# Performance work log

Hardware: AMD Instinct MI355X
Metric: run time of the kernel (lower is better)

The kernel has to match this reference:

```python
import jax, jax.numpy as jnp
import numpy as np

B, N, D = 1, 2048, 1024
L, H, DH = 4, 16, 64
INNER = H * DH            # 1024, == D
FF = int(D * 4.0)         # 4096 (GEGLU inner)
SCALE = DH ** -0.5
LN_EPS = 1e-5


def setup_inputs() -> dict:
    key = jax.random.key(0)
    ks = jax.random.split(key, 8)
    w = 0.02
    inp = {
        'x': jax.random.normal(ks[0], (B, N, D), jnp.float32),
        'mask': jnp.ones((B, N), dtype=bool),
        # stacked per-layer params (leading dim L)
        'Wqkv': jax.random.normal(ks[1], (L, D, 3 * INNER), jnp.float32) * w,
        'Wo': jax.random.normal(ks[2], (L, INNER, D), jnp.float32) * w,
        'bo': jnp.zeros((L, D), jnp.float32),
        'ln1_g': jnp.ones((L, D), jnp.float32),
        'ln1_b': jnp.zeros((L, D), jnp.float32),
        'ln2_g': jnp.ones((L, D), jnp.float32),
        'ln2_b': jnp.zeros((L, D), jnp.float32),
        'ls1': jnp.full((L, D), 0.1, jnp.float32),  # LayerScale init_eps=0.1 (depth<=18)
        'ls2': jnp.full((L, D), 0.1, jnp.float32),
        'W1': jax.random.normal(ks[3], (L, D, 2 * FF), jnp.float32) * w,
        'b1': jnp.zeros((L, 2 * FF), jnp.float32),
        'W2': jax.random.normal(ks[4], (L, FF, D), jnp.float32) * w,
        'b2': jnp.zeros((L, D), jnp.float32),
    }
    return inp


def _layernorm(x, g, b):
    mu = jnp.mean(x, axis=-1, keepdims=True)
    var = jnp.mean(jnp.square(x - mu), axis=-1, keepdims=True)
    return (x - mu) * jax.lax.rsqrt(var + LN_EPS) * g + b


def _forward(x, mask, Wqkv, Wo, bo, ln1_g, ln1_b, ln2_g, ln2_b, ls1, ls2, W1, b1, W2, b2):
    n = x.shape[1]
    causal = jnp.arange(n)[None, :] > jnp.arange(n)[:, None]  # True = masked
    valid = mask[:, None, None, :] & ~causal[None, None]       # (B,1,N,N) True = keep
    for l in range(L):
        # --- attention sublayer: x + LayerScale(PreNorm(Attn))(x) ---
        h = _layernorm(x, ln1_g[l], ln1_b[l])
        qkv = h @ Wqkv[l]                                      # (B,N,3*INNER)
        q, k, v = jnp.split(qkv, 3, axis=-1)
        q = q.reshape(B, n, H, DH).transpose(0, 2, 1, 3) * SCALE
        k = k.reshape(B, n, H, DH).transpose(0, 2, 1, 3)
        v = v.reshape(B, n, H, DH).transpose(0, 2, 1, 3)
        dots = jnp.einsum('bhid,bhjd->bhij', q, k)             # (B,H,N,N)
        neg = -jnp.finfo(dots.dtype).max
        dots = jnp.where(valid, dots, neg)
        attn = jax.nn.softmax(dots, axis=-1)                   # stable_softmax, temp=1
        o = jnp.einsum('bhij,bhjd->bhid', attn, v)
        o = o.transpose(0, 2, 1, 3).reshape(B, n, INNER)
        o = o @ Wo[l] + bo[l]
        x = x + o * ls1[l]
        # --- feedforward sublayer: x + LayerScale(PreNorm(GEGLU-FFN))(x) ---
        h = _layernorm(x, ln2_g[l], ln2_b[l])
        u = h @ W1[l] + b1[l]                                  # (B,N,2*FF)
        a, g = jnp.split(u, 2, axis=-1)
        f = (a * jax.nn.gelu(g, approximate=False)) @ W2[l] + b2[l]
        x = x + f * ls2[l]
    return x


def reference(x, mask, Wqkv, Wo, bo, ln1_g, ln1_b, ln2_g, ln2_b, ls1, ls2, W1, b1, W2, b2):
    return _forward(x, mask, Wqkv, Wo, bo, ln1_g, ln1_b, ln2_g, ln2_b, ls1, ls2, W1, b1, W2, b2)
```

## Files before the change

### kernel.cpp

```cpp
#include <hip/hip_runtime.h>
#include <hip/hip_bf16.h>
#include <math.h>

#define LN_EPS 1e-5f
#define ATT_SCALE 0.125f

typedef __bf16 bf16x8 __attribute__((ext_vector_type(8)));
typedef float f32x4 __attribute__((ext_vector_type(4)));

__device__ __forceinline__ unsigned short f2bf(float f){
  unsigned int u = __builtin_bit_cast(unsigned int, f);
  u += 0x7fffu + ((u >> 16) & 1u);
  return (unsigned short)(u >> 16);
}
__device__ __forceinline__ float bfbits2f(unsigned int lo16){
  return __builtin_bit_cast(float, lo16 << 16);
}

__global__ __launch_bounds__(256) void ln_kernel(
    const float* __restrict__ X, const float* __restrict__ g,
    const float* __restrict__ b, unsigned short* __restrict__ H)
{
  __shared__ float red[4];
  int row = blockIdx.x, t = threadIdx.x;
  const float4 xv = ((const float4*)(X + (size_t)row*1024))[t];
  float s = xv.x + xv.y + xv.z + xv.w;
  #pragma unroll
  for (int o=32;o;o>>=1) s += __shfl_down(s,o);
  if ((t&63)==0) red[t>>6] = s;
  __syncthreads();
  float mu = (red[0]+red[1]+red[2]+red[3]) * (1.f/1024.f);
  __syncthreads();
  float dx = xv.x-mu, dy = xv.y-mu, dz = xv.z-mu, dw = xv.w-mu;
  float s2 = dx*dx+dy*dy+dz*dz+dw*dw;
  #pragma unroll
  for (int o=32;o;o>>=1) s2 += __shfl_down(s2,o);
  if ((t&63)==0) red[t>>6] = s2;
  __syncthreads();
  float var = (red[0]+red[1]+red[2]+red[3]) * (1.f/1024.f);
  float rs = rsqrtf(var + LN_EPS);
  const float4 gv = ((const float4*)g)[t];
  const float4 bv = ((const float4*)b)[t];
  ushort4 o4;
  o4.x = f2bf(dx*rs*gv.x + bv.x);
  o4.y = f2bf(dy*rs*gv.y + bv.y);
  o4.z = f2bf(dz*rs*gv.z + bv.z);
  o4.w = f2bf(dw*rs*gv.w + bv.w);
  ((ushort4*)(H + (size_t)row*1024))[t] = o4;
}

template<int SK, int DO_LN>
__global__ __launch_bounds__(256) void redln_kernel(
    const float* __restrict__ P, float* __restrict__ X,
    const float* __restrict__ bias, const float* __restrict__ scale,
    const float* __restrict__ g, const float* __restrict__ b,
    unsigned short* __restrict__ H)
{
  __shared__ float red[4];
  int row = blockIdx.x, t = threadIdx.x;
  size_t off = (size_t)row*1024 + t*4;
  float4 xv = *(const float4*)(X + off);
  float4 pv = *(const float4*)(P + off);
  #pragma unroll
  for (int c=1;c<SK;c++){
    float4 q = *(const float4*)(P + (size_t)c*2048*1024 + off);
    pv.x+=q.x; pv.y+=q.y; pv.z+=q.z; pv.w+=q.w;
  }
  const float4 bv = ((const float4*)bias)[t];
  const float4 sv = ((const float4*)scale)[t];
  xv.x += (pv.x+bv.x)*sv.x;
  xv.y += (pv.y+bv.y)*sv.y;
  xv.z += (pv.z+bv.z)*sv.z;
  xv.w += (pv.w+bv.w)*sv.w;
  *(float4*)(X + off) = xv;
  if (DO_LN){
    float s = xv.x + xv.y + xv.z + xv.w;
    #pragma unroll
    for (int o=32;o;o>>=1) s += __shfl_down(s,o);
    if ((t&63)==0) red[t>>6] = s;
    __syncthreads();
    float mu = (red[0]+red[1]+red[2]+red[3]) * (1.f/1024.f);
    __syncthreads();
    float dx = xv.x-mu, dy = xv.y-mu, dz = xv.z-mu, dw = xv.w-mu;
    float s2 = dx*dx+dy*dy+dz*dz+dw*dw;
    #pragma unroll
    for (int o=32;o;o>>=1) s2 += __shfl_down(s2,o);
    if ((t&63)==0) red[t>>6] = s2;
    __syncthreads();
    float var = (red[0]+red[1]+red[2]+red[3]) * (1.f/1024.f);
    float rs = rsqrtf(var + LN_EPS);
    const float4 gv = ((const float4*)g)[t];
    const float4 lbv = ((const float4*)b)[t];
    ushort4 o4;
    o4.x = f2bf(dx*rs*gv.x + lbv.x);
    o4.y = f2bf(dy*rs*gv.y + lbv.y);
    o4.z = f2bf(dz*rs*gv.z + lbv.z);
    o4.w = f2bf(dw*rs*gv.w + lbv.w);
    ((ushort4*)(H + (size_t)row*1024))[t] = o4;
  }
}

__global__ __launch_bounds__(256) void trc_kernel(
    const float* __restrict__ W, unsigned short* __restrict__ WT, int K, int N)
{
  __shared__ float tile[64][65];
  int n0 = blockIdx.x*64, k0 = blockIdx.y*64;
  int t = threadIdx.x;
  int tx = t & 63, ty = t >> 6;
  #pragma unroll
  for (int p=0;p<16;p++){
    int r = ty*16+p;
    tile[r][tx] = W[(size_t)(k0+r)*N + n0 + tx];
  }
  __syncthreads();
  int kc = t & 31, tb = t >> 5;
  #pragma unroll
  for (int p=0;p<8;p++){
    int nr = tb + p*8;
    unsigned int lo = f2bf(tile[2*kc][nr]);
    unsigned int hi = f2bf(tile[2*kc+1][nr]);
    ((unsigned int*)(WT + (size_t)(n0+nr)*K + k0))[kc] = lo | (hi<<16);
  }
}

template<int MODE>
__global__ __launch_bounds__(256) void gemm_bt(
    const unsigned short* __restrict__ A, const unsigned short* __restrict__ BT,
    int M, int N, int K,
    float* __restrict__ Xres, unsigned short* __restrict__ Obf,
    const float* __restrict__ bias, const float* __restrict__ scale)
{
  __shared__ unsigned short Asm[128*64];
  __shared__ unsigned short Bsm[128*64];
  int t = threadIdx.x;
  int lane = t & 63;
  int w = t >> 6, wm = w >> 1, wn = w & 1;

  int nwg = gridDim.x * gridDim.y;
  int wg = blockIdx.y * gridDim.x + blockIdx.x;
  int cpx = nwg >> 3;
  int swz = (wg & 7) * cpx + (wg >> 3);
  int bn = swz % gridDim.x, bm = swz / gridDim.x;

  f32x4 acc[4][4] = {};
  int ktBeg = 0, ktEnd = K >> 6;
  if (MODE == 3){
    int per = (K >> 6) / gridDim.z;
    ktBeg = blockIdx.z * per;
    ktEnd = ktBeg + per;
  }

  for (int kt = ktBeg; kt < ktEnd; ++kt){
    #pragma unroll
    for (int c=0;c<4;c++){
      int li = c*256 + t;
      int row = li >> 3, sc = li & 7;
      int gc = sc ^ (row & 7);
      const unsigned short* sa = A  + (size_t)(bm*128 + row)*K + kt*64 + gc*8;
      const unsigned short* sb = BT + (size_t)(bn*128 + row)*K + kt*64 + gc*8;
      __builtin_amdgcn_global_load_lds(
        (const __attribute__((address_space(1))) unsigned int*)sa,
        (__attribute__((address_space(3))) unsigned int*)(Asm + (size_t)(c*256 + (t & ~63))*8),
        16, 0, 0);
      __builtin_amdgcn_global_load_lds(
        (const __attribute__((address_space(1))) unsigned int*)sb,
        (__attribute__((address_space(3))) unsigned int*)(Bsm + (size_t)(c*256 + (t & ~63))*8),
        16, 0, 0);
    }
    __syncthreads();
    #pragma unroll
    for (int kk=0;kk<2;kk++){
      bf16x8 aF[4], bF[4];
      #pragma unroll
      for (int m=0;m<4;m++){
        int row = wm*64 + m*16 + (lane&15);
        int ch = kk*4 + (lane>>4);
        aF[m] = *(const bf16x8*)&Asm[row*64 + (ch ^ (row&7))*8];
      }
      #pragma unroll
      for (int n=0;n<4;n++){
        int row = wn*64 + n*16 + (lane&15);
        int ch = kk*4 + (lane>>4);
        bF[n] = *(const bf16x8*)&Bsm[row*64 + (ch ^ (row&7))*8];
      }
      #pragma unroll
      for (int m=0;m<4;m++)
        #pragma unroll
        for (int n=0;n<4;n++)
          acc[m][n] = __builtin_amdgcn_mfma_f32_16x16x32_bf16(aF[m], bF[n], acc[m][n], 0,0,0);
    }
    __syncthreads();
  }

  int colg = lane & 15;
  #pragma unroll
  for (int m=0;m<4;m++){
    int gr0 = bm*128 + wm*64 + m*16 + (lane>>4)*4;
    #pragma unroll
    for (int n=0;n<4;n++){
      int gc = bn*128 + wn*64 + n*16 + colg;
      #pragma unroll
      for (int j=0;j<4;j++){
        int gr = gr0 + j;
        float v = acc[m][n][j];
        if (MODE==0){
          Obf[(size_t)gr*N + gc] = f2bf(v);
        } else if (MODE==1){
          Obf[(size_t)gr*N + gc] = f2bf(v + bias[gc]);
        } else if (MODE==2){
          size_t idx = (size_t)gr*N + gc;
          Xres[idx] = Xres[idx] + (v + bias[gc]) * scale[gc];
        } else {
          Xres[(size_t)blockIdx.z*((size_t)M*N) + (size_t)gr*N + gc] = v;
        }
      }
    }
  }
}

__global__ __launch_bounds__(256) void vtr_kernel(
    const unsigned short* __restrict__ qkv, unsigned short* __restrict__ VT)
{
  __shared__ unsigned int tile[64][33];
  int h = blockIdx.y;
  int n0 = blockIdx.x * 64;
  int t = threadIdx.x;
  #pragma unroll
  for (int p=0;p<8;p++){
    int idx = p*256 + t;
    int r = idx >> 5, c = idx & 31;
    tile[r][c] = *(const unsigned int*)(qkv + (size_t)(n0+r)*3072 + 2048 + h*64 + c*2);
  }
  __syncthreads();
  #pragma unroll
  for (int p=0;p<8;p++){
    int idx = p*256 + t;
    int d = idx >> 5, c = idx & 31;
    unsigned int a = tile[2*c][d>>1];
    unsigned int b = tile[2*c+1][d>>1];
    unsigned int lo = (d&1) ? (a>>16) : (a & 0xffffu);
    unsigned int hi = (d&1) ? (b>>16) : (b & 0xffffu);
    *(unsigned int*)(VT + (size_t)h*131072 + (size_t)d*2048 + n0 + c*2) = lo | (hi<<16);
  }
}

__global__ __launch_bounds__(256) void flash_attn(
    const unsigned short* __restrict__ qkv,
    const unsigned short* __restrict__ VT,
    unsigned short* __restrict__ O)
{
  __shared__ unsigned short Klds[64*64];
  __shared__ unsigned short Vlds[64*64];
  __shared__ unsigned short Plds[4][16*72];
  __shared__ float fbuf[4][16];
  __shared__ float lbuf[4][16];

  int t = threadIdx.x;
  int lane = t & 63;
  int w = t >> 6;
  int q15 = lane & 15, l16 = lane >> 4;

  int bid = blockIdx.x;
  int half = bid >> 8, idx = bid & 255;
  int h = (idx >> 5) + half*8;
  int qt = half ? (31 - (idx & 31)) : (idx & 31);
  int q0 = qt * 64;

  bf16x8 qF[2];
  int qrow = q0 + w*16 + q15;
  #pragma unroll
  for (int db=0; db<2; db++)
    qF[db] = *(const bf16x8*)(qkv + (size_t)qrow*3072 + h*64 + db*32 + l16*8);

  f32x4 o[4] = {};
  float m_run = -1e30f, l_run = 0.f;

  for (int kt = 0; kt <= qt; ++kt){
    int k0 = kt*64;
    #pragma unroll
    for (int c=0;c<2;c++){
      int li = c*256 + t;
      int row = li >> 3, sc = li & 7;
      int gc = sc ^ (row & 7);
      const unsigned short* sk = qkv + (size_t)(k0+row)*3072 + 1024 + h*64 + gc*8;
      const unsigned short* sv = VT + (size_t)h*131072 + (size_t)row*2048 + k0 + gc*8;
      __builtin_amdgcn_global_load_lds(
        (const __attribute__((address_space(1))) unsigned int*)sk,
        (__attribute__((address_space(3))) unsigned int*)(Klds + (c*256 + (t & ~63))*8),
        16, 0, 0);
      __builtin_amdgcn_global_load_lds(
        (const __attribute__((address_space(1))) unsigned int*)sv,
        (__attribute__((address_space(3))) unsigned int*)(Vlds + (c*256 + (t & ~63))*8),
        16, 0, 0);
    }
    __syncthreads();

    f32x4 s[4] = {};
    #pragma unroll
    for (int km=0;km<4;km++){
      #pragma unroll
      for (int db=0;db<2;db++){
        int row = km*16 + q15;
        int ch = db*4 + l16;
        bf16x8 kF = *(const bf16x8*)&Klds[row*64 + (ch ^ (row&7))*8];
        s[km] = __builtin_amdgcn_mfma_f32_16x16x32_bf16(kF, qF[db], s[km], 0,0,0);
      }
    }

    bool diag = (kt == qt);
    float pmax = -1e30f;
    #pragma unroll
    for (int km=0;km<4;km++){
      #pragma unroll
      for (int j=0;j<4;j++){
        float sv = s[km][j] * ATT_SCALE;
        if (diag){
          int kg = km*16 + l16*4 + j;
          int qg = w*16 + q15;
          if (kg > qg) sv = -1e30f;
        }
        s[km][j] = sv;
        pmax = fmaxf(pmax, sv);
      }
    }
    pmax = fmaxf(pmax, __shfl_xor(pmax, 16));
    pmax = fmaxf(pmax, __shfl_xor(pmax, 32));

    float m_new = fmaxf(m_run, pmax);
    float f = __expf(m_run - m_new);

    float lsum = 0.f;
    #pragma unroll
    for (int km=0;km<4;km++){
      float p0 = __expf(s[km][0]-m_new);
      float p1 = __expf(s[km][1]-m_new);
      float p2 = __expf(s[km][2]-m_new);
      float p3 = __expf(s[km][3]-m_new);
      lsum += (p0+p1)+(p2+p3);
      unsigned int u0 = (unsigned int)f2bf(p0) | ((unsigned int)f2bf(p1)<<16);
      unsigned int u1 = (unsigned int)f2bf(p2) | ((unsigned int)f2bf(p3)<<16);
      *(uint2*)&Plds[w][q15*72 + km*16 + l16*4] = make_uint2(u0,u1);
    }
    lsum += __shfl_xor(lsum,16);
    lsum += __shfl_xor(lsum,32);
    l_run = l_run * f + lsum;
    m_run = m_new;

    if (l16 == 0) fbuf[w][q15] = f;
    f32x4 fv = *(f32x4*)&fbuf[w][l16*4];
    #pragma unroll
    for (int n=0;n<4;n++) o[n] *= fv;

    #pragma unroll
    for (int kb=0;kb<2;kb++){
      bf16x8 aP = *(const bf16x8*)&Plds[w][q15*72 + kb*32 + l16*8];
      #pragma unroll
      for (int n=0;n<4;n++){
        int row = n*16 + q15;
        int ch = kb*4 + l16;
        bf16x8 vF = *(const bf16x8*)&Vlds[row*64 + (ch ^ (row&7))*8];
        o[n] = __builtin_amdgcn_mfma_f32_16x16x32_bf16(aP, vF, o[n], 0,0,0);
      }
    }
    __syncthreads();
  }

  if (l16 == 0) lbuf[w][q15] = 1.f / l_run;
  f32x4 lv = *(f32x4*)&lbuf[w][l16*4];

  #pragma unroll
  for (int n=0;n<4;n++){
    #pragma unroll
    for (int j=0;j<4;j++){
      int row = q0 + w*16 + l16*4 + j;
      int col = h*64 + n*16 + q15;
      O[(size_t)row*1024 + col] = f2bf(o[n][j]*lv[j]);
    }
  }
}

__global__ __launch_bounds__(256) void geglu_kernel(
    const unsigned short* __restrict__ U, unsigned short* __restrict__ F)
{
  int v = blockIdx.x*256 + threadIdx.x;
  int r = v >> 9, c8 = v & 511;
  const uint4 av = *(const uint4*)(U + (size_t)r*8192 + c8*8);
  const uint4 gv = *(const uint4*)(U + (size_t)r*8192 + 4096 + c8*8);
  unsigned int aw[4] = {av.x,av.y,av.z,av.w};
  unsigned int gw[4] = {gv.x,gv.y,gv.z,gv.w};
  unsigned int ow[4];
  #pragma unroll
  for (int c=0;c<4;c++){
    float a0 = bfbits2f(aw[c]&0xffffu), a1 = bfbits2f(aw[c]>>16);
    float g0 = bfbits2f(gw[c]&0xffffu), g1 = bfbits2f(gw[c]>>16);
    float f0 = a0 * 0.5f * g0 * (1.f + erff(g0*0.70710678118f));
    float f1 = a1 * 0.5f * g1 * (1.f + erff(g1*0.70710678118f));
    ow[c] = (unsigned int)f2bf(f0) | ((unsigned int)f2bf(f1)<<16);
  }
  *(uint4*)(F + (size_t)r*4096 + c8*8) = make_uint4(ow[0],ow[1],ow[2],ow[3]);
}

extern "C" void kernel_launch(void* const* d_in, const int* in_sizes, int n_in,
                              void* d_out, int out_size, void* d_ws, size_t ws_size,
                              hipStream_t stream)
{
  (void)in_sizes; (void)n_in; (void)out_size; (void)ws_size;
  const float* x_in = (const float*)d_in[0];
  const float* Wqkv = (const float*)d_in[2];
  const float* Wo   = (const float*)d_in[3];
  const float* bo   = (const float*)d_in[4];
  const float* ln1g = (const float*)d_in[5];
  const float* ln1b = (const float*)d_in[6];
  const float* ln2g = (const float*)d_in[7];
  const float* ln2b = (const float*)d_in[8];
  const float* ls1  = (const float*)d_in[9];
  const float* ls2  = (const float*)d_in[10];
  const float* W1   = (const float*)d_in[11];
  const float* b1   = (const float*)d_in[12];
  const float* W2   = (const float*)d_in[13];
  const float* b2   = (const float*)d_in[14];
  float* X = (float*)d_out;

  char* ws = (char*)d_ws;
  unsigned short* WT = (unsigned short*)(ws);
  unsigned short* hb = (unsigned short*)(ws + (16u<<20));
  unsigned short* qu = (unsigned short*)(ws + (20u<<20));
  unsigned short* of = (unsigned short*)(ws + (52u<<20));
  unsigned short* VTg = (unsigned short*)(ws + (36u<<20));
  float* PT = (float*)(ws + (20u<<20));

  hipMemcpyAsync(d_out, (const void*)x_in, (size_t)2048*1024*4,
                 hipMemcpyDeviceToDevice, stream);

  for (int l = 0; l < 4; ++l){
    if (l == 0)
      ln_kernel<<<2048,256,0,stream>>>(X, ln1g, ln1b, hb);
    trc_kernel<<<dim3(3072/64,1024/64),256,0,stream>>>(Wqkv + (size_t)l*1024*3072, WT, 1024, 3072);
    gemm_bt<0><<<dim3(3072/128,2048/128),256,0,stream>>>(hb, WT, 2048,3072,1024,
        nullptr, qu, nullptr, nullptr);
    vtr_kernel<<<dim3(32,16),256,0,stream>>>(qu, VTg);
    flash_attn<<<512,256,0,stream>>>(qu, VTg, of);
    trc_kernel<<<dim3(1024/64,1024/64),256,0,stream>>>(Wo + (size_t)l*1024*1024, WT, 1024, 1024);
    gemm_bt<3><<<dim3(1024/128,2048/128,2),256,0,stream>>>(of, WT, 2048,1024,1024,
        PT, nullptr, nullptr, nullptr);
    redln_kernel<2,1><<<2048,256,0,stream>>>(PT, X, bo + l*1024, ls1 + l*1024,
        ln2g + l*1024, ln2b + l*1024, hb);
    trc_kernel<<<dim3(8192/64,1024/64),256,0,stream>>>(W1 + (size_t)l*1024*8192, WT, 1024, 8192);
    gemm_bt<1><<<dim3(8192/128,2048/128),256,0,stream>>>(hb, WT, 2048,8192,1024,
        nullptr, qu, b1 + l*8192, nullptr);
    geglu_kernel<<<4096,256,0,stream>>>(qu, of);
    trc_kernel<<<dim3(1024/64,4096/64),256,0,stream>>>(W2 + (size_t)l*4096*1024, WT, 4096, 1024);
    gemm_bt<3><<<dim3(1024/128,2048/128,4),256,0,stream>>>(of, WT, 2048,1024,4096,
        PT, nullptr, nullptr, nullptr);
    if (l < 3)
      redln_kernel<4,1><<<2048,256,0,stream>>>(PT, X, b2 + l*1024, ls2 + l*1024,
          ln1g + (l+1)*1024, ln1b + (l+1)*1024, hb);
    else
      redln_kernel<4,0><<<2048,256,0,stream>>>(PT, X, b2 + l*1024, ls2 + l*1024,
          nullptr, nullptr, nullptr);
  }
}
```

Measured before the change: 887.7 us.

## Fuse GEGLU into W1 GEMM with interleaved weight layout and 256-tile pipelined GEMM

Adds a new 256x256-tile GEMM that stages tiles into LDS with direct global-to-LDS loads through a three-buffer pipeline. The W1 transpose interleaves the a and gate columns so each wave holds matching pairs, which lets the GEGLU bias and erf-gelu run in the GEMM epilogue. This removes the separate geglu kernel and the bf16 round trip of the 2048x8192 intermediate. The W2 GEMM uses the new kernel with split-K 8 when the workspace is large enough, which costs a wider partial-sum reduction in redln.

```diff
diff --git a/kernel.cpp b/kernel.cpp
--- a/kernel.cpp
+++ b/kernel.cpp
@@ -7,6 +7,8 @@
 
 typedef __bf16 bf16x8 __attribute__((ext_vector_type(8)));
 typedef float f32x4 __attribute__((ext_vector_type(4)));
+
+#define VWAIT(N) asm volatile("s_waitcnt vmcnt(" #N ")" ::: "memory")
 
 __device__ __forceinline__ unsigned short f2bf(float f){
   unsigned int u = __builtin_bit_cast(unsigned int, f);
@@ -120,6 +122,33 @@
     unsigned int lo = f2bf(tile[2*kc][nr]);
     unsigned int hi = f2bf(tile[2*kc+1][nr]);
     ((unsigned int*)(WT + (size_t)(n0+nr)*K + k0))[kc] = lo | (hi<<16);
+  }
+}
+
+__global__ __launch_bounds__(256) void trc_w1_kernel(
+    const float* __restrict__ W, unsigned short* __restrict__ WT)
+{
+  __shared__ float tile[64][65];
+  int n0 = blockIdx.x*64, k0 = blockIdx.y*64;
+  int ca = (n0>>5)*16;
+  int t = threadIdx.x;
+  int tx = t & 63, ty = t >> 6;
+  #pragma unroll
+  for (int p=0;p<16;p++){
+    int r = ty*16+p;
+    int col = (tx < 32) ? (ca + tx) : (ca + 4064 + tx);
+    tile[r][tx] = W[(size_t)(k0+r)*8192 + col];
+  }
+  __syncthreads();
+  int kc = t & 31, tb = t >> 5;
+  #pragma unroll
+  for (int p=0;p<8;p++){
+    int nr = tb + p*8;
+    int rr = nr & 31;
+    int vcol = (nr>>5)*16 + (rr&15) + ((rr>>4)<<5);
+    unsigned int lo = f2bf(tile[2*kc][vcol]);
+    unsigned int hi = f2bf(tile[2*kc+1][vcol]);
+    ((unsigned int*)(WT + (size_t)(n0+nr)*1024 + k0))[kc] = lo | (hi<<16);
   }
 }
 
@@ -205,14 +234,143 @@
         float v = acc[m][n][j];
         if (MODE==0){
           Obf[(size_t)gr*N + gc] = f2bf(v);
-        } else if (MODE==1){
-          Obf[(size_t)gr*N + gc] = f2bf(v + bias[gc]);
-        } else if (MODE==2){
-          size_t idx = (size_t)gr*N + gc;
-          Xres[idx] = Xres[idx] + (v + bias[gc]) * scale[gc];
         } else {
           Xres[(size_t)blockIdx.z*((size_t)M*N) + (size_t)gr*N + gc] = v;
         }
+      }
+    }
+  }
+}
+
+template<int MODE>
+__global__ __launch_bounds__(512,2) void gemm256(
+    const unsigned short* __restrict__ A, const unsigned short* __restrict__ BT,
+    int M, int N, int K,
+    float* __restrict__ Pout, unsigned short* __restrict__ Fout,
+    const float* __restrict__ b1)
+{
+  __shared__ unsigned short lds[3*16384];
+  int t = threadIdx.x;
+  int lane = t & 63;
+  int w = t >> 6;
+  int wm = w >> 2, wn = w & 3;
+  int colg = lane & 15, l16 = lane >> 4;
+
+  int nwg = gridDim.x * gridDim.y;
+  int wg = blockIdx.y * gridDim.x + blockIdx.x;
+  int cpx = nwg >> 3;
+  int swz = (wg & 7) * cpx + (wg >> 3);
+  int bn = swz % gridDim.x, bm = swz / gridDim.x;
+
+  int nktTot = K >> 5;
+  int nkt = (MODE==3) ? (nktTot / gridDim.z) : nktTot;
+  int ktBeg = (MODE==3) ? (blockIdx.z * nkt) : 0;
+
+  int rA0 = bm*256, rB0 = bn*256;
+
+  int offA[8], offB[4];
+  #pragma unroll
+  for (int m=0;m<8;m++){
+    int row = wm*128 + m*16 + colg;
+    offA[m] = row*32 + (l16 ^ ((row>>1)&3))*8;
+  }
+  #pragma unroll
+  for (int n=0;n<4;n++){
+    int row = wn*64 + n*16 + colg;
+    offB[n] = 8192 + row*32 + (l16 ^ ((row>>1)&3))*8;
+  }
+
+  f32x4 acc[8][4] = {};
+
+  auto STAGE = [&](int kt, int buf){
+    unsigned short* bp = lds + buf*16384;
+    #pragma unroll
+    for (int l=0;l<2;l++){
+      int ci = l*512 + t;
+      int row = ci>>2, slot = ci&3;
+      int gc = slot ^ ((row>>1)&3);
+      const unsigned short* sa = A  + (size_t)(rA0+row)*K + (ktBeg+kt)*32 + gc*8;
+      const unsigned short* sb = BT + (size_t)(rB0+row)*K + (ktBeg+kt)*32 + gc*8;
+      __builtin_amdgcn_global_load_lds(
+        (const __attribute__((address_space(1))) unsigned int*)sa,
+        (__attribute__((address_space(3))) unsigned int*)(bp + (l*512 + (t&~63))*8),
+        16, 0, 0);
+      __builtin_amdgcn_global_load_lds(
+        (const __attribute__((address_space(1))) unsigned int*)sb,
+        (__attribute__((address_space(3))) unsigned int*)(bp + 8192 + (l*512 + (t&~63))*8),
+        16, 0, 0);
+    }
+  };
+
+  auto COMPUTE = [&](int buf){
+    const unsigned short* bp = lds + buf*16384;
+    bf16x8 aF[8], bF[4];
+    #pragma unroll
+    for (int m=0;m<8;m++) aF[m] = *(const bf16x8*)(bp + offA[m]);
+    #pragma unroll
+    for (int n=0;n<4;n++) bF[n] = *(const bf16x8*)(bp + offB[n]);
+    __builtin_amdgcn_s_setprio(1);
+    #pragma unroll
+    for (int m=0;m<8;m++)
+      #pragma unroll
+      for (int n=0;n<4;n++)
+        acc[m][n] = __builtin_amdgcn_mfma_f32_16x16x32_bf16(aF[m], bF[n], acc[m][n], 0,0,0);
+    __builtin_amdgcn_s_setprio(0);
+  };
+
+  STAGE(0,0); STAGE(1,1);
+  int cur = 0, stg = 2;
+  for (int kt = 0; kt < nkt-2; ++kt){
+    STAGE(kt+2, stg);
+    VWAIT(8);
+    __builtin_amdgcn_s_barrier();
+    COMPUTE(cur);
+    __builtin_amdgcn_s_barrier();
+    int oc = cur; cur = (cur==2)?0:cur+1; stg = oc;
+  }
+  VWAIT(4);
+  __builtin_amdgcn_s_barrier();
+  COMPUTE(cur);
+  __builtin_amdgcn_s_barrier();
+  cur = (cur==2)?0:cur+1;
+  VWAIT(0);
+  __builtin_amdgcn_s_barrier();
+  COMPUTE(cur);
+
+  if (MODE==4){
+    float b1a[2], b1g[2];
+    #pragma unroll
+    for (int p=0;p<2;p++){
+      int oc = (bn*8 + wn*2 + p)*16 + colg;
+      b1a[p] = b1[oc];
+      b1g[p] = b1[oc + 4096];
+    }
+    #pragma unroll
+    for (int m=0;m<8;m++){
+      int gr0 = bm*256 + wm*128 + m*16 + l16*4;
+      #pragma unroll
+      for (int p=0;p<2;p++){
+        int ocol = (bn*8 + wn*2 + p)*16 + colg;
+        #pragma unroll
+        for (int j=0;j<4;j++){
+          float va = acc[m][2*p][j]   + b1a[p];
+          float vg = acc[m][2*p+1][j] + b1g[p];
+          float f = va * (0.5f * vg * (1.f + erff(vg * 0.70710678118f)));
+          Fout[(size_t)(gr0+j)*4096 + ocol] = f2bf(f);
+        }
+      }
+    }
+  } else {
+    size_t zoff = (size_t)blockIdx.z * ((size_t)M*N);
+    #pragma unroll
+    for (int m=0;m<8;m++){
+      int gr0 = bm*256 + wm*128 + m*16 + l16*4;
+      #pragma unroll
+      for (int n=0;n<4;n++){
+        int gc = bn*256 + wn*64 + n*16 + colg;
+        #pragma unroll
+        for (int j=0;j<4;j++)
+          Pout[zoff + (size_t)(gr0+j)*N + gc] = acc[m][n][j];
       }
     }
   }
@@ -379,32 +537,11 @@
   }
 }
 
-__global__ __launch_bounds__(256) void geglu_kernel(
-    const unsigned short* __restrict__ U, unsigned short* __restrict__ F)
-{
-  int v = blockIdx.x*256 + threadIdx.x;
-  int r = v >> 9, c8 = v & 511;
-  const uint4 av = *(const uint4*)(U + (size_t)r*8192 + c8*8);
-  const uint4 gv = *(const uint4*)(U + (size_t)r*8192 + 4096 + c8*8);
-  unsigned int aw[4] = {av.x,av.y,av.z,av.w};
-  unsigned int gw[4] = {gv.x,gv.y,gv.z,gv.w};
-  unsigned int ow[4];
-  #pragma unroll
-  for (int c=0;c<4;c++){
-    float a0 = bfbits2f(aw[c]&0xffffu), a1 = bfbits2f(aw[c]>>16);
-    float g0 = bfbits2f(gw[c]&0xffffu), g1 = bfbits2f(gw[c]>>16);
-    float f0 = a0 * 0.5f * g0 * (1.f + erff(g0*0.70710678118f));
-    float f1 = a1 * 0.5f * g1 * (1.f + erff(g1*0.70710678118f));
-    ow[c] = (unsigned int)f2bf(f0) | ((unsigned int)f2bf(f1)<<16);
-  }
-  *(uint4*)(F + (size_t)r*4096 + c8*8) = make_uint4(ow[0],ow[1],ow[2],ow[3]);
-}
-
 extern "C" void kernel_launch(void* const* d_in, const int* in_sizes, int n_in,
                               void* d_out, int out_size, void* d_ws, size_t ws_size,
                               hipStream_t stream)
 {
-  (void)in_sizes; (void)n_in; (void)out_size; (void)ws_size;
+  (void)in_sizes; (void)n_in; (void)out_size;
   const float* x_in = (const float*)d_in[0];
   const float* Wqkv = (const float*)d_in[2];
   const float* Wo   = (const float*)d_in[3];
@@ -422,12 +559,14 @@
   float* X = (float*)d_out;
 
   char* ws = (char*)d_ws;
-  unsigned short* WT = (unsigned short*)(ws);
-  unsigned short* hb = (unsigned short*)(ws + (16u<<20));
-  unsigned short* qu = (unsigned short*)(ws + (20u<<20));
-  unsigned short* of = (unsigned short*)(ws + (52u<<20));
+  unsigned short* WT  = (unsigned short*)(ws);
+  unsigned short* hb  = (unsigned short*)(ws + (16u<<20));
+  unsigned short* qu  = (unsigned short*)(ws + (20u<<20));
   unsigned short* VTg = (unsigned short*)(ws + (36u<<20));
-  float* PT = (float*)(ws + (20u<<20));
+  unsigned short* of  = (unsigned short*)(ws + (52u<<20));
+  float* PT  = (float*)(ws + (20u<<20));
+  float* PT8 = (float*)(ws + (68u<<20));
+  const bool big = ws_size >= (134ull<<20);
 
   hipMemcpyAsync(d_out, (const void*)x_in, (size_t)2048*1024*4,
                  hipMemcpyDeviceToDevice, stream);
@@ -445,18 +584,28 @@
         PT, nullptr, nullptr, nullptr);
     redln_kernel<2,1><<<2048,256,0,stream>>>(PT, X, bo + l*1024, ls1 + l*1024,
         ln2g + l*1024, ln2b + l*1024, hb);
-    trc_kernel<<<dim3(8192/64,1024/64),256,0,stream>>>(W1 + (size_t)l*1024*8192, WT, 1024, 8192);
-    gemm_bt<1><<<dim3(8192/128,2048/128),256,0,stream>>>(hb, WT, 2048,8192,1024,
-        nullptr, qu, b1 + l*8192, nullptr);
-    geglu_kernel<<<4096,256,0,stream>>>(qu, of);
+    trc_w1_kernel<<<dim3(8192/64,1024/64),256,0,stream>>>(W1 + (size_t)l*1024*8192, WT);
+    gemm256<4><<<dim3(8192/256,2048/256),512,0,stream>>>(hb, WT, 2048,8192,1024,
+        nullptr, of, b1 + (size_t)l*8192);
     trc_kernel<<<dim3(1024/64,4096/64),256,0,stream>>>(W2 + (size_t)l*4096*1024, WT, 4096, 1024);
-    gemm_bt<3><<<dim3(1024/128,2048/128,4),256,0,stream>>>(of, WT, 2048,1024,4096,
-        PT, nullptr, nullptr, nullptr);
-    if (l < 3)
-      redln_kernel<4,1><<<2048,256,0,stream>>>(PT, X, b2 + l*1024, ls2 + l*1024,
-          ln1g + (l+1)*1024, ln1b + (l+1)*1024, hb);
-    else
-      redln_kernel<4,0><<<2048,256,0,stream>>>(PT, X, b2 + l*1024, ls2 + l*1024,
-          nullptr, nullptr, nullptr);
-  }
-}
+    if (big){
+      gemm256<3><<<dim3(1024/256,2048/256,8),512,0,stream>>>(of, WT, 2048,1024,4096,
+          PT8, nullptr, nullptr);
+      if (l < 3)
+        redln_kernel<8,1><<<2048,256,0,stream>>>(PT8, X, b2 + l*1024, ls2 + l*1024,
+            ln1g + (l+1)*1024, ln1b + (l+1)*1024, hb);
+      else
+        redln_kernel<8,0><<<2048,256,0,stream>>>(PT8, X, b2 + l*1024, ls2 + l*1024,
+            nullptr, nullptr, nullptr);
+    } else {
+      gemm_bt<3><<<dim3(1024/128,2048/128,4),256,0,stream>>>(of, WT, 2048,1024,4096,
+          PT, nullptr, nullptr, nullptr);
+      if (l < 3)
+        redln_kernel<4,1><<<2048,256,0,stream>>>(PT, X, b2 + l*1024, ls2 + l*1024,
+            ln1g + (l+1)*1024, ln1b + (l+1)*1024, hb);
+      else
+        redln_kernel<4,0><<<2048,256,0,stream>>>(PT, X, b2 + l*1024, ls2 + l*1024,
+            nullptr, nullptr, nullptr);
+    }
+  }
+}
```

Measured after the change: 846.4 us. 1.05x faster.

## Fuse GEGLU into W1 GEMM epilogue via interleaved weight transpose

Applied to the files above, without the earlier changes.

The W1 weight transpose now interleaves value and gate columns in 16-wide groups, so each output tile of the W1 GEMM holds matching value and gate halves. A new GEMM epilogue mode applies the bias and exact-erf GELU gating and writes the 4096-wide bf16 result straight to the FFN activation buffer. This removes the separate GEGLU kernel and the write and re-read of the 2048x8192 intermediate. In exchange the GEMM epilogue does more math and stores only half as many columns, and the index remapping has to match the transpose layout exactly.

```diff
diff --git a/kernel.cpp b/kernel.cpp
--- a/kernel.cpp
+++ b/kernel.cpp
@@ -120,6 +120,33 @@
     unsigned int lo = f2bf(tile[2*kc][nr]);
     unsigned int hi = f2bf(tile[2*kc+1][nr]);
     ((unsigned int*)(WT + (size_t)(n0+nr)*K + k0))[kc] = lo | (hi<<16);
+  }
+}
+
+__global__ __launch_bounds__(256) void trc_w1_kernel(
+    const float* __restrict__ W, unsigned short* __restrict__ WT)
+{
+  __shared__ float tile[64][65];
+  int n0 = blockIdx.x*64, k0 = blockIdx.y*64;
+  int ca = (n0>>5)*16;
+  int t = threadIdx.x;
+  int tx = t & 63, ty = t >> 6;
+  #pragma unroll
+  for (int p=0;p<16;p++){
+    int r = ty*16+p;
+    int col = (tx < 32) ? (ca + tx) : (ca + 4064 + tx);
+    tile[r][tx] = W[(size_t)(k0+r)*8192 + col];
+  }
+  __syncthreads();
+  int kc = t & 31, tb = t >> 5;
+  #pragma unroll
+  for (int p=0;p<8;p++){
+    int nr = tb + p*8;
+    int rr = nr & 31;
+    int vcol = (nr>>5)*16 + (rr&15) + ((rr>>4)<<5);
+    unsigned int lo = f2bf(tile[2*kc][vcol]);
+    unsigned int hi = f2bf(tile[2*kc+1][vcol]);
+    ((unsigned int*)(WT + (size_t)(n0+nr)*1024 + k0))[kc] = lo | (hi<<16);
   }
 }
 
@@ -193,6 +220,31 @@
   }
 
   int colg = lane & 15;
+  if (MODE==4){
+    float b1a[2], b1g[2];
+    #pragma unroll
+    for (int p=0;p<2;p++){
+      int oc = (bn*4 + wn*2 + p)*16 + colg;
+      b1a[p] = bias[oc];
+      b1g[p] = bias[oc + 4096];
+    }
+    #pragma unroll
+    for (int m=0;m<4;m++){
+      int gr0 = bm*128 + wm*64 + m*16 + (lane>>4)*4;
+      #pragma unroll
+      for (int p=0;p<2;p++){
+        int ocol = (bn*4 + wn*2 + p)*16 + colg;
+        #pragma unroll
+        for (int j=0;j<4;j++){
+          float va = acc[m][2*p][j]   + b1a[p];
+          float vg = acc[m][2*p+1][j] + b1g[p];
+          float f = va * (0.5f * vg * (1.f + erff(vg * 0.70710678118f)));
+          Obf[(size_t)(gr0+j)*4096 + ocol] = f2bf(f);
+        }
+      }
+    }
+    return;
+  }
   #pragma unroll
   for (int m=0;m<4;m++){
     int gr0 = bm*128 + wm*64 + m*16 + (lane>>4)*4;
@@ -205,11 +257,6 @@
         float v = acc[m][n][j];
         if (MODE==0){
           Obf[(size_t)gr*N + gc] = f2bf(v);
-        } else if (MODE==1){
-          Obf[(size_t)gr*N + gc] = f2bf(v + bias[gc]);
-        } else if (MODE==2){
-          size_t idx = (size_t)gr*N + gc;
-          Xres[idx] = Xres[idx] + (v + bias[gc]) * scale[gc];
         } else {
           Xres[(size_t)blockIdx.z*((size_t)M*N) + (size_t)gr*N + gc] = v;
         }
@@ -377,27 +424,6 @@
       O[(size_t)row*1024 + col] = f2bf(o[n][j]*lv[j]);
     }
   }
-}
-
-__global__ __launch_bounds__(256) void geglu_kernel(
-    const unsigned short* __restrict__ U, unsigned short* __restrict__ F)
-{
-  int v = blockIdx.x*256 + threadIdx.x;
-  int r = v >> 9, c8 = v & 511;
-  const uint4 av = *(const uint4*)(U + (size_t)r*8192 + c8*8);
-  const uint4 gv = *(const uint4*)(U + (size_t)r*8192 + 4096 + c8*8);
-  unsigned int aw[4] = {av.x,av.y,av.z,av.w};
-  unsigned int gw[4] = {gv.x,gv.y,gv.z,gv.w};
-  unsigned int ow[4];
-  #pragma unroll
-  for (int c=0;c<4;c++){
-    float a0 = bfbits2f(aw[c]&0xffffu), a1 = bfbits2f(aw[c]>>16);
-    float g0 = bfbits2f(gw[c]&0xffffu), g1 = bfbits2f(gw[c]>>16);
-    float f0 = a0 * 0.5f * g0 * (1.f + erff(g0*0.70710678118f));
-    float f1 = a1 * 0.5f * g1 * (1.f + erff(g1*0.70710678118f));
-    ow[c] = (unsigned int)f2bf(f0) | ((unsigned int)f2bf(f1)<<16);
-  }
-  *(uint4*)(F + (size_t)r*4096 + c8*8) = make_uint4(ow[0],ow[1],ow[2],ow[3]);
 }
 
 extern "C" void kernel_launch(void* const* d_in, const int* in_sizes, int n_in,
@@ -422,12 +448,12 @@
   float* X = (float*)d_out;
 
   char* ws = (char*)d_ws;
-  unsigned short* WT = (unsigned short*)(ws);
-  unsigned short* hb = (unsigned short*)(ws + (16u<<20));
-  unsigned short* qu = (unsigned short*)(ws + (20u<<20));
-  unsigned short* of = (unsigned short*)(ws + (52u<<20));
+  unsigned short* WT  = (unsigned short*)(ws);
+  unsigned short* hb  = (unsigned short*)(ws + (16u<<20));
+  unsigned short* qu  = (unsigned short*)(ws + (20u<<20));
   unsigned short* VTg = (unsigned short*)(ws + (36u<<20));
-  float* PT = (float*)(ws + (20u<<20));
+  unsigned short* of  = (unsigned short*)(ws + (52u<<20));
+  float* PT  = (float*)(ws + (20u<<20));
 
   hipMemcpyAsync(d_out, (const void*)x_in, (size_t)2048*1024*4,
                  hipMemcpyDeviceToDevice, stream);
@@ -445,10 +471,9 @@
         PT, nullptr, nullptr, nullptr);
     redln_kernel<2,1><<<2048,256,0,stream>>>(PT, X, bo + l*1024, ls1 + l*1024,
         ln2g + l*1024, ln2b + l*1024, hb);
-    trc_kernel<<<dim3(8192/64,1024/64),256,0,stream>>>(W1 + (size_t)l*1024*8192, WT, 1024, 8192);
-    gemm_bt<1><<<dim3(8192/128,2048/128),256,0,stream>>>(hb, WT, 2048,8192,1024,
-        nullptr, qu, b1 + l*8192, nullptr);
-    geglu_kernel<<<4096,256,0,stream>>>(qu, of);
+    trc_w1_kernel<<<dim3(8192/64,1024/64),256,0,stream>>>(W1 + (size_t)l*1024*8192, WT);
+    gemm_bt<4><<<dim3(8192/128,2048/128),256,0,stream>>>(hb, WT, 2048,8192,1024,
+        nullptr, of, b1 + (size_t)l*8192, nullptr);
     trc_kernel<<<dim3(1024/64,4096/64),256,0,stream>>>(W2 + (size_t)l*4096*1024, WT, 4096, 1024);
     gemm_bt<3><<<dim3(1024/128,2048/128,4),256,0,stream>>>(of, WT, 2048,1024,4096,
         PT, nullptr, nullptr, nullptr);
```

Result: slower. 914.1 us (+3.0%).
